# Optimization experiments

Measured on AMD Instinct MI355X. Metric: run time of the kernel, lower is better.

Reference implementation:

```python
import jax, jax.numpy as jnp
import numpy as np
import math

N_LAYER = 4
D = 1024
H = 16
V = 32000
MAX_LEN = 2048
B = 2
L = 2048
EPS = 1e-6


def positional_encoding(max_len, dim):
    pos = jnp.arange(max_len, dtype=jnp.float32)[:, None]
    div = jnp.exp(jnp.arange(0, dim, 2, dtype=jnp.float32) * (-math.log(10000.0) / dim))
    ang = pos * div  # [max_len, dim//2]
    pe = jnp.zeros((max_len, dim), dtype=jnp.float32)
    pe = pe.at[:, 0::2].set(jnp.sin(ang)).at[:, 1::2].set(jnp.cos(ang))
    return pe


def setup_inputs() -> dict:
    key = jax.random.key(0)
    ks = jax.random.split(key, 20)
    s = 0.02
    inp = {
        "input_ids": jax.random.randint(ks[0], (B, L), 0, V),
        "embed": jax.random.normal(ks[1], (V, D), jnp.float32) * s,
        "Wq": jax.random.normal(ks[2], (N_LAYER, D, D), jnp.float32) * s,
        "bq": jnp.zeros((N_LAYER, D), jnp.float32),
        "Wk": jax.random.normal(ks[3], (N_LAYER, D, D), jnp.float32) * s,
        "bk": jnp.zeros((N_LAYER, D), jnp.float32),
        "Wv": jax.random.normal(ks[4], (N_LAYER, D, D), jnp.float32) * s,
        "bv": jnp.zeros((N_LAYER, D), jnp.float32),
        "Wo": jax.random.normal(ks[5], (N_LAYER, D, D), jnp.float32) * s,
        "bo": jnp.zeros((N_LAYER, D), jnp.float32),
        "Wproj": jax.random.normal(ks[6], (N_LAYER, D, 2 * D), jnp.float32) * s,
        "bproj": jnp.zeros((N_LAYER, 2 * D), jnp.float32),
        "Wup": jax.random.normal(ks[7], (N_LAYER, D, 2 * D), jnp.float32) * s,
        "bup": jnp.zeros((N_LAYER, 2 * D), jnp.float32),
        "Wdown": jax.random.normal(ks[8], (N_LAYER, 2 * D, D), jnp.float32) * s,
        "bdown": jnp.zeros((N_LAYER, D), jnp.float32),
        "gammas": jnp.ones((2 * N_LAYER, D), jnp.float32),
        "Wlogits": jax.random.normal(ks[9], (D, V), jnp.float32) * s,
        "blogits": jnp.zeros((V,), jnp.float32),
    }
    return inp


def rmsnorm(x, gamma):
    ms = jnp.mean(x * x, axis=-1, keepdims=True)
    return x * jax.lax.rsqrt(ms + EPS) * gamma


def attention(x, Wq, bq, Wk, bk, Wv, bv, Wo, bo):
    b, l, d = x.shape
    dh = d // H
    q = (x @ Wq + bq).reshape(b, l, H, dh)
    k = (x @ Wk + bk).reshape(b, l, H, dh)
    v = (x @ Wv + bv).reshape(b, l, H, dh)
    scores = jnp.einsum("blhd,bmhd->bhlm", q, k) / math.sqrt(dh)
    causal = jnp.tril(jnp.ones((l, l), dtype=bool))  # True where allowed
    scores = jnp.where(causal, scores, -jnp.inf)
    attn = jax.nn.softmax(scores, axis=-1)
    out = jnp.einsum("bhlm,bmhd->blhd", attn, v).reshape(b, l, d)
    return out @ Wo + bo


def ffn(x, Wproj, bproj, Wup, bup, Wdown, bdown):
    proj = x @ Wproj + bproj
    up = x @ Wup + bup
    gate = jax.nn.silu(proj * up)
    return gate @ Wdown + bdown


def reference(input_ids, embed, Wq, bq, Wk, bk, Wv, bv, Wo, bo,
              Wproj, bproj, Wup, bup, Wdown, bdown, gammas, Wlogits, blogits):
    b, l = input_ids.shape
    pe = positional_encoding(MAX_LEN, D)[:l]
    x = embed[input_ids] + pe
    for i in range(N_LAYER):
        x = x + attention(rmsnorm(x, gammas[2 * i]),
                          Wq[i], bq[i], Wk[i], bk[i], Wv[i], bv[i], Wo[i], bo[i])
        x = x + ffn(rmsnorm(x, gammas[2 * i + 1]),
                    Wproj[i], bproj[i], Wup[i], bup[i], Wdown[i], bdown[i])
    return x @ Wlogits + blogits
```

## Files before the change

### kernel.cpp

```cpp
#include <hip/hip_runtime.h>


typedef _Float16 f16;
typedef _Float16 v8h __attribute__((ext_vector_type(8)));
typedef float    v4f __attribute__((ext_vector_type(4)));

#define B_   2
#define L_   2048
#define D_   1024
#define H_   16
#define V_   32000
#define M_   (B_ * L_)

__device__ inline void g2l16(const void* g, void* l) {
  __builtin_amdgcn_global_load_lds((const __attribute__((address_space(1))) void*)g,
                                   (__attribute__((address_space(3))) void*)l,
                                   16, 0, 0);
}

__device__ inline void xcd_swz(int& bx, int& by, int gx, int gy) {
  int nwg  = gx * gy;
  int orig = by * gx + bx;
  int q = nwg >> 3, r = nwg & 7;
  int xcd = orig & 7, local = orig >> 3;
  int swz = (xcd < r ? xcd * (q + 1) : r * (q + 1) + (xcd - r) * q) + local;
  bx = swz % gx;
  by = swz / gx;
}

template<int EPI>
__global__ __launch_bounds__(256) void gemm_bt(
    const f16* __restrict__ A, const f16* __restrict__ Bt,
    const float* __restrict__ bias, const float* resid, void* outp,
    int N, int K)
{
  __shared__ alignas(16) f16 As[128 * 32];
  __shared__ alignas(16) f16 Bs[128 * 32];

  int bx = blockIdx.x, by = blockIdx.y;
  xcd_swz(bx, by, (int)gridDim.x, (int)gridDim.y);

  const int tid  = threadIdx.x;
  const int wave = tid >> 6, lane = tid & 63;
  const int quad = lane >> 4, l16 = lane & 15;
  const long tm = (long)bx * 128;
  const long tn = (long)by * 128;
  const int wm = (wave >> 1) * 64, wn = (wave & 1) * 64;

  v4f acc[4][4];
  for (int i = 0; i < 4; ++i)
    for (int j = 0; j < 4; ++j)
      for (int r = 0; r < 4; ++r) acc[i][j][r] = 0.f;

  for (int k0 = 0; k0 < K; k0 += 32) {
    __syncthreads();
    for (int h = 0; h < 2; ++h) {
      int c = h * 256 + wave * 64 + lane;
      long row = c >> 2;
      long koff = (long)k0 + (c & 3) * 8;
      g2l16(A  + (tm + row) * K + koff, As + (h * 256 + wave * 64) * 8);
      g2l16(Bt + (tn + row) * K + koff, Bs + (h * 256 + wave * 64) * 8);
    }
    __syncthreads();

    v8h a[4], b[4];
    for (int i = 0; i < 4; ++i) {
      a[i] = *(const v8h*)(As + (wm + i * 16 + l16) * 32 + quad * 8);
      b[i] = *(const v8h*)(Bs + (wn + i * 16 + l16) * 32 + quad * 8);
    }
    for (int i = 0; i < 4; ++i)
      for (int j = 0; j < 4; ++j)
        acc[i][j] = __builtin_amdgcn_mfma_f32_16x16x32_f16(a[i], b[j], acc[i][j], 0, 0, 0);
  }

  for (int i = 0; i < 4; ++i)
    for (int r = 0; r < 4; ++r) {
      long row = tm + wm + i * 16 + quad * 4 + r;
      for (int j = 0; j < 4; ++j) {
        long col = tn + wn + j * 16 + l16;
        float v = acc[i][j][r] + bias[col];
        long idx = row * (long)N + col;
        if (EPI == 0)      ((f16*)outp)[idx] = (f16)v;
        else if (EPI == 1) ((float*)outp)[idx] = resid[idx] + v;
        else               ((float*)outp)[idx] = v;
      }
    }
}

template<int EPI>
__global__ __launch_bounds__(256) void gemm64_bt(
    const f16* __restrict__ A, const f16* __restrict__ Bt,
    const float* __restrict__ bias, const float* resid, void* outp,
    int N, int K)
{
  __shared__ alignas(16) f16 As[128 * 32];
  __shared__ alignas(16) f16 Bs[64 * 32];

  int bx = blockIdx.x, by = blockIdx.y;
  xcd_swz(bx, by, (int)gridDim.x, (int)gridDim.y);

  const int tid  = threadIdx.x;
  const int wave = tid >> 6, lane = tid & 63;
  const int quad = lane >> 4, l16 = lane & 15;
  const long tm = (long)bx * 128;
  const long tn = (long)by * 64;
  const int wm = (wave >> 1) * 64, wn = (wave & 1) * 32;

  v4f acc[4][2];
  for (int i = 0; i < 4; ++i)
    for (int j = 0; j < 2; ++j)
      for (int r = 0; r < 4; ++r) acc[i][j][r] = 0.f;

  for (int k0 = 0; k0 < K; k0 += 32) {
    __syncthreads();
    for (int h = 0; h < 2; ++h) {
      int c = h * 256 + wave * 64 + lane;
      long row = c >> 2;
      long koff = (long)k0 + (c & 3) * 8;
      g2l16(A + (tm + row) * K + koff, As + (h * 256 + wave * 64) * 8);
    }
    {
      int c = wave * 64 + lane;
      long row = c >> 2;
      long koff = (long)k0 + (c & 3) * 8;
      g2l16(Bt + (tn + row) * K + koff, Bs + (wave * 64) * 8);
    }
    __syncthreads();

    v8h a[4], b[2];
    for (int i = 0; i < 4; ++i)
      a[i] = *(const v8h*)(As + (wm + i * 16 + l16) * 32 + quad * 8);
    for (int j = 0; j < 2; ++j)
      b[j] = *(const v8h*)(Bs + (wn + j * 16 + l16) * 32 + quad * 8);
    for (int i = 0; i < 4; ++i)
      for (int j = 0; j < 2; ++j)
        acc[i][j] = __builtin_amdgcn_mfma_f32_16x16x32_f16(a[i], b[j], acc[i][j], 0, 0, 0);
  }

  for (int i = 0; i < 4; ++i)
    for (int r = 0; r < 4; ++r) {
      long row = tm + wm + i * 16 + quad * 4 + r;
      for (int j = 0; j < 2; ++j) {
        long col = tn + wn + j * 16 + l16;
        float v = acc[i][j][r] + bias[col];
        long idx = row * (long)N + col;
        if (EPI == 0)      ((f16*)outp)[idx] = (f16)v;
        else if (EPI == 1) ((float*)outp)[idx] = resid[idx] + v;
        else               ((float*)outp)[idx] = v;
      }
    }
}

__global__ __launch_bounds__(256) void attn_k(const f16* __restrict__ qkv,
                                              f16* __restrict__ attno)
{
  const int qt = (int)gridDim.x - 1 - blockIdx.x;
  const int bh = blockIdx.y;
  const int b = bh >> 4, h = bh & 15;
  const int tid = threadIdx.x;
  const int wave = tid >> 6, lane = tid & 63;
  const int quad = lane >> 4, l16 = lane & 15;

  __shared__ alignas(16) f16 Ks[32 * 64];
  __shared__ alignas(16) f16 Vt[64 * 32];
  __shared__ alignas(16) f16 Ps[4][16 * 32];

  const f16* base = qkv + (size_t)b * L_ * 3072 + h * 64;

  const int qrow = qt * 64 + wave * 16 + l16;
  const v8h qf0 = *(const v8h*)(base + (size_t)qrow * 3072 + quad * 8);
  const v8h qf1 = *(const v8h*)(base + (size_t)qrow * 3072 + 32 + quad * 8);

  v4f of[4];
  float m_i[4], l_i[4];
  for (int n = 0; n < 4; ++n)
    for (int r = 0; r < 4; ++r) of[n][r] = 0.f;
  for (int r = 0; r < 4; ++r) { m_i[r] = -1e30f; l_i[r] = 0.f; }

  const int kr = tid >> 3, kc = tid & 7;
  const int vkr = tid & 31, vkc = tid >> 5;
  const int nblocks = qt * 2 + 2;

  for (int kb = 0; kb < nblocks; ++kb) {
    const int key0 = kb * 32;
    __syncthreads();
    {
      const f16* ksrc = base + 1024 + (size_t)(key0 + kr) * 3072 + kc * 8;
      *(v8h*)(Ks + kr * 64 + ((kc ^ (kr & 7)) * 8)) = *(const v8h*)ksrc;
      const f16* vsrc = base + 2048 + (size_t)(key0 + vkr) * 3072 + vkc * 8;
      v8h vv = *(const v8h*)vsrc;
      const int vc = vkr >> 3, vs = vkr & 7;
      for (int e = 0; e < 8; ++e) {
        int row = vkc * 8 + e;
        Vt[row * 32 + ((vc ^ ((row >> 1) & 3)) * 8) + vs] = vv[e];
      }
    }
    __syncthreads();

    v4f sf[2];
    for (int s = 0; s < 2; ++s)
      for (int r = 0; r < 4; ++r) sf[s][r] = 0.f;
    for (int s = 0; s < 2; ++s) {
      int row = s * 16 + l16;
      v8h kf0 = *(const v8h*)(Ks + row * 64 + ((quad ^ (row & 7)) * 8));
      v8h kf1 = *(const v8h*)(Ks + row * 64 + (((4 + quad) ^ (row & 7)) * 8));
      sf[s] = __builtin_amdgcn_mfma_f32_16x16x32_f16(qf0, kf0, sf[s], 0, 0, 0);
      sf[s] = __builtin_amdgcn_mfma_f32_16x16x32_f16(qf1, kf1, sf[s], 0, 0, 0);
    }

    const int qg0 = qt * 64 + wave * 16 + quad * 4;
    float pv[2][4];
    for (int s = 0; s < 2; ++s)
      for (int r = 0; r < 4; ++r) {
        float sc = sf[s][r] * 0.125f;
        int kg = key0 + s * 16 + l16;
        if (kg > qg0 + r) sc = -1e30f;
        pv[s][r] = sc;
      }

    for (int r = 0; r < 4; ++r) {
      float mx = fmaxf(pv[0][r], pv[1][r]);
      for (int o = 8; o; o >>= 1) mx = fmaxf(mx, __shfl_xor(mx, o, 64));
      float mnew = fmaxf(m_i[r], mx);
      float alpha = expf(m_i[r] - mnew);
      m_i[r] = mnew;
      pv[0][r] = expf(pv[0][r] - mnew);
      pv[1][r] = expf(pv[1][r] - mnew);
      float rs = pv[0][r] + pv[1][r];
      for (int o = 8; o; o >>= 1) rs += __shfl_xor(rs, o, 64);
      l_i[r] = l_i[r] * alpha + rs;
      for (int n = 0; n < 4; ++n) of[n][r] *= alpha;
      Ps[wave][(quad * 4 + r) * 32 + l16]      = (f16)pv[0][r];
      Ps[wave][(quad * 4 + r) * 32 + 16 + l16] = (f16)pv[1][r];
    }
    __syncthreads();

    v8h pf = *(const v8h*)(&Ps[wave][0] + l16 * 32 + quad * 8);
    for (int n = 0; n < 4; ++n) {
      int vrow = n * 16 + l16;
      v8h vf = *(const v8h*)(Vt + vrow * 32 + ((quad ^ ((vrow >> 1) & 3)) * 8));
      of[n] = __builtin_amdgcn_mfma_f32_16x16x32_f16(pf, vf, of[n], 0, 0, 0);
    }
  }

  const int q = qt * 64 + wave * 16 + quad * 4;
  f16* orow = attno + (size_t)b * L_ * 1024 + h * 64;
  for (int r = 0; r < 4; ++r) {
    float inv = 1.0f / l_i[r];
    for (int n = 0; n < 4; ++n)
      orow[(size_t)(q + r) * 1024 + n * 16 + l16] = (f16)(of[n][r] * inv);
  }
}

__global__ __launch_bounds__(256) void embed_pe(const int* __restrict__ ids,
                                                const float* __restrict__ emb,
                                                float* __restrict__ x)
{
  const int bl = blockIdx.x;
  const int l = bl & (L_ - 1);
  const int id = ids[bl];
  const float* e = emb + (size_t)id * D_;
  float* xr = x + (size_t)bl * D_;
  const int d0 = threadIdx.x * 4;
  for (int i = 0; i < 4; ++i) {
    int d = d0 + i;
    int p = d >> 1;
    float ang = (float)l * expf((float)(2 * p) * -0.008994473019508053f);
    float pe = (d & 1) ? cosf(ang) : sinf(ang);
    xr[d] = e[d] + pe;
  }
}

__global__ __launch_bounds__(256) void rmsnorm_k(const float* __restrict__ x,
                                                 const float* __restrict__ gamma,
                                                 f16* __restrict__ y)
{
  const int row = blockIdx.x;
  const float4 v = ((const float4*)(x + (size_t)row * D_))[threadIdx.x];
  float s = v.x * v.x + v.y * v.y + v.z * v.z + v.w * v.w;
  for (int o = 32; o; o >>= 1) s += __shfl_xor(s, o, 64);
  __shared__ float red[4];
  const int wave = threadIdx.x >> 6;
  if ((threadIdx.x & 63) == 0) red[wave] = s;
  __syncthreads();
  const float tot = red[0] + red[1] + red[2] + red[3];
  const float scale = rsqrtf(tot * (1.0f / D_) + 1e-6f);
  f16* yr = y + (size_t)row * D_;
  const int d = threadIdx.x * 4;
  yr[d]     = (f16)(v.x * scale * gamma[d]);
  yr[d + 1] = (f16)(v.y * scale * gamma[d + 1]);
  yr[d + 2] = (f16)(v.z * scale * gamma[d + 2]);
  yr[d + 3] = (f16)(v.w * scale * gamma[d + 3]);
}

__global__ __launch_bounds__(256) void transpose_cvt(const float* __restrict__ in,
                                                     f16* __restrict__ out,
                                                     int K, int N)
{
  __shared__ float tile[32][33];
  const int r = threadIdx.x >> 5, c = threadIdx.x & 31;
  const size_t bk = (size_t)blockIdx.y * 32;
  const size_t bn = (size_t)blockIdx.x * 32;
  for (int i = 0; i < 32; i += 8)
    tile[r + i][c] = in[(bk + r + i) * N + bn + c];
  __syncthreads();
  for (int i = 0; i < 32; i += 8)
    out[(bn + r + i) * K + bk + c] = (f16)tile[c][r + i];
}

__global__ __launch_bounds__(256) void gate_k(const f16* __restrict__ PU,
                                              f16* __restrict__ g)
{
  const int e = (blockIdx.x * 256 + threadIdx.x) * 4;
  const int row = e >> 11, col = e & 2047;
  const f16* p = PU + (size_t)row * 4096 + col;
  const f16* u = p + 2048;
  f16* go = g + (size_t)row * 2048 + col;
  for (int i = 0; i < 4; ++i) {
    float z = (float)p[i] * (float)u[i];
    go[i] = (f16)(z / (1.0f + expf(-z)));
  }
}

__global__ __launch_bounds__(256) void cast_k(const float* __restrict__ x,
                                              f16* __restrict__ y)
{
  const int i = blockIdx.x * 1024 + threadIdx.x * 4;
  const float4 v = *(const float4*)(x + i);
  y[i] = (f16)v.x; y[i + 1] = (f16)v.y; y[i + 2] = (f16)v.z; y[i + 3] = (f16)v.w;
}

__global__ __launch_bounds__(256) void build_biases(
    const float* bq, const float* bk, const float* bv,
    const float* bp, const float* bu, float* bqkv, float* bpu)
{
  const int i = blockIdx.x;
  for (int j = threadIdx.x; j < 3072; j += 256)
    bqkv[i * 3072 + j] = j < 1024 ? bq[i * 1024 + j]
                       : j < 2048 ? bk[i * 1024 + j - 1024]
                                  : bv[i * 1024 + j - 2048];
  for (int j = threadIdx.x; j < 4096; j += 256)
    bpu[i * 4096 + j] = j < 2048 ? bp[i * 2048 + j] : bu[i * 2048 + j - 2048];
}

extern "C" void kernel_launch(void* const* d_in, const int* in_sizes, int n_in,
                              void* d_out, int out_size, void* d_ws, size_t ws_size,
                              hipStream_t stream)
{
  (void)in_sizes; (void)n_in; (void)out_size; (void)ws_size;
  const int*   ids     = (const int*)  d_in[0];
  const float* embed   = (const float*)d_in[1];
  const float* Wq      = (const float*)d_in[2];
  const float* bq      = (const float*)d_in[3];
  const float* Wk      = (const float*)d_in[4];
  const float* bk      = (const float*)d_in[5];
  const float* Wv      = (const float*)d_in[6];
  const float* bv      = (const float*)d_in[7];
  const float* Wo      = (const float*)d_in[8];
  const float* bo      = (const float*)d_in[9];
  const float* Wproj   = (const float*)d_in[10];
  const float* bproj   = (const float*)d_in[11];
  const float* Wup     = (const float*)d_in[12];
  const float* bup     = (const float*)d_in[13];
  const float* Wdown   = (const float*)d_in[14];
  const float* bdown   = (const float*)d_in[15];
  const float* gammas  = (const float*)d_in[16];
  const float* Wlogits = (const float*)d_in[17];
  const float* blogits = (const float*)d_in[18];

  char* ws = (char*)d_ws;
  float* x    = (float*)ws;
  f16*   y    = (f16*)  (ws + 16777216);
  float* bqkv = (float*)(ws + 25165824);
  float* bpu  = (float*)(ws + 25214976);
  f16*   wbuf = (f16*)  (ws + 25280512);
  f16* wqkvT  = wbuf;
  f16* woT    = wbuf + 3145728;
  f16* wpuT   = wbuf + 4194304;
  f16* wdownT = wbuf + 8388608;

  char* ob  = (char*)d_out;
  f16* qkv   = (f16*)ob;
  f16* attno = (f16*)(ob + 25165824);
  f16* PU    = (f16*)(ob + 33554432);
  f16* g     = (f16*)(ob + 67108864);

  embed_pe<<<M_, 256, 0, stream>>>(ids, embed, x);
  build_biases<<<4, 256, 0, stream>>>(bq, bk, bv, bproj, bup, bqkv, bpu);

  for (int i = 0; i < 4; ++i) {
    const float* Wqi = Wq + (size_t)i * 1048576;
    const float* Wki = Wk + (size_t)i * 1048576;
    const float* Wvi = Wv + (size_t)i * 1048576;
    const float* Woi = Wo + (size_t)i * 1048576;
    const float* Wpi = Wproj + (size_t)i * 2097152;
    const float* Wui = Wup   + (size_t)i * 2097152;
    const float* Wdi = Wdown + (size_t)i * 2097152;

    transpose_cvt<<<dim3(32, 32), 256, 0, stream>>>(Wqi, wqkvT,                1024, 1024);
    transpose_cvt<<<dim3(32, 32), 256, 0, stream>>>(Wki, wqkvT + 1048576,      1024, 1024);
    transpose_cvt<<<dim3(32, 32), 256, 0, stream>>>(Wvi, wqkvT + 2097152,      1024, 1024);
    transpose_cvt<<<dim3(32, 32), 256, 0, stream>>>(Woi, woT,                  1024, 1024);
    transpose_cvt<<<dim3(64, 32), 256, 0, stream>>>(Wpi, wpuT,                 1024, 2048);
    transpose_cvt<<<dim3(64, 32), 256, 0, stream>>>(Wui, wpuT + 2097152,       1024, 2048);
    transpose_cvt<<<dim3(32, 64), 256, 0, stream>>>(Wdi, wdownT,               2048, 1024);

    rmsnorm_k<<<M_, 256, 0, stream>>>(x, gammas + (size_t)(2 * i) * 1024, y);
    gemm_bt<0><<<dim3(32, 24), 256, 0, stream>>>(y, wqkvT, bqkv + i * 3072, nullptr, qkv, 3072, 1024);
    attn_k<<<dim3(32, 32), 256, 0, stream>>>(qkv, attno);
    gemm64_bt<1><<<dim3(32, 16), 256, 0, stream>>>(attno, woT, bo + i * 1024, x, x, 1024, 1024);

    rmsnorm_k<<<M_, 256, 0, stream>>>(x, gammas + (size_t)(2 * i + 1) * 1024, y);
    gemm_bt<0><<<dim3(32, 32), 256, 0, stream>>>(y, wpuT, bpu + i * 4096, nullptr, PU, 4096, 1024);
    gate_k<<<8192, 256, 0, stream>>>(PU, g);
    gemm64_bt<1><<<dim3(32, 16), 256, 0, stream>>>(g, wdownT, bdown + i * 1024, x, x, 1024, 2048);
  }

  transpose_cvt<<<dim3(1000, 32), 256, 0, stream>>>(Wlogits, wbuf, 1024, 32000);
  cast_k<<<M_, 256, 0, stream>>>(x, y);
  gemm_bt<2><<<dim3(32, 250), 256, 0, stream>>>(y, wbuf, blogits, nullptr, (float*)d_out, 32000, 1024);
}
```

Before: 2.756 ms.

## Enlarge GEMM tiles to 256x128, swizzle LDS, group tile mapping, widen attention key blocks

The main GEMM moves from 128x128 to 256x128 tiles, so each wave does 8x4 MFMAs per k-step and operands are reused more. Both GEMM kernels now apply an XOR swizzle to LDS rows to avoid bank conflicts, and a grouped, XCD-aware tile mapping improves L2 locality. The attention kernel processes 64 keys per block instead of 32, loads K straight into LDS asynchronously, and uses swizzled layouts for V and P. The larger accumulator raises register pressure and occupancy is capped by launch bounds. With 16x24 blocks the QKV GEMM may leave some CUs idle.

```diff
diff --git a/kernel.cpp b/kernel.cpp
--- a/kernel.cpp
+++ b/kernel.cpp
@@ -18,62 +18,76 @@
                                    16, 0, 0);
 }
 
-__device__ inline void xcd_swz(int& bx, int& by, int gx, int gy) {
-  int nwg  = gx * gy;
-  int orig = by * gx + bx;
-  int q = nwg >> 3, r = nwg & 7;
-  int xcd = orig & 7, local = orig >> 3;
-  int swz = (xcd < r ? xcd * (q + 1) : r * (q + 1) + (xcd - r) * q) + local;
-  bx = swz % gx;
-  by = swz / gx;
+__device__ inline void tile_map(int& m, int& n) {
+  const int GX = (int)gridDim.x, GY = (int)gridDim.y;
+  const int nwg = GX * GY;
+  const int flat = (int)(blockIdx.y * gridDim.x + blockIdx.x);
+  const int per = nwg >> 3, r = nwg & 7;
+  const int xcd = flat & 7, lo = flat >> 3;
+  const int swz = (xcd < r ? xcd * (per + 1) : r * (per + 1) + (xcd - r) * per) + lo;
+  const int MG = 4;
+  const int band = swz / (MG * GY), rem = swz % (MG * GY);
+  n = rem / MG;
+  m = band * MG + (rem % MG);
 }
 
 template<int EPI>
-__global__ __launch_bounds__(256) void gemm_bt(
+__global__ __launch_bounds__(256, 2) void gemm_wt(
     const f16* __restrict__ A, const f16* __restrict__ Bt,
     const float* __restrict__ bias, const float* resid, void* outp,
     int N, int K)
 {
-  __shared__ alignas(16) f16 As[128 * 32];
+  __shared__ alignas(16) f16 As[256 * 32];
   __shared__ alignas(16) f16 Bs[128 * 32];
 
-  int bx = blockIdx.x, by = blockIdx.y;
-  xcd_swz(bx, by, (int)gridDim.x, (int)gridDim.y);
+  int bm, bn;
+  tile_map(bm, bn);
 
   const int tid  = threadIdx.x;
   const int wave = tid >> 6, lane = tid & 63;
   const int quad = lane >> 4, l16 = lane & 15;
-  const long tm = (long)bx * 128;
-  const long tn = (long)by * 128;
-  const int wm = (wave >> 1) * 64, wn = (wave & 1) * 64;
-
-  v4f acc[4][4];
-  for (int i = 0; i < 4; ++i)
+  const long tm = (long)bm * 256;
+  const long tn = (long)bn * 128;
+  const int wm = (wave >> 1) * 128, wn = (wave & 1) * 64;
+
+  v4f acc[8][4];
+  for (int i = 0; i < 8; ++i)
     for (int j = 0; j < 4; ++j)
       for (int r = 0; r < 4; ++r) acc[i][j][r] = 0.f;
 
   for (int k0 = 0; k0 < K; k0 += 32) {
     __syncthreads();
+    for (int h = 0; h < 4; ++h) {
+      int c = h * 256 + tid;
+      long row = c >> 2;
+      int jslot = c & 3;
+      long koff = (long)k0 + ((jslot ^ ((row >> 1) & 3)) << 3);
+      g2l16(A + (tm + row) * K + koff, As + (h * 256 + wave * 64) * 8);
+    }
     for (int h = 0; h < 2; ++h) {
-      int c = h * 256 + wave * 64 + lane;
+      int c = h * 256 + tid;
       long row = c >> 2;
-      long koff = (long)k0 + (c & 3) * 8;
-      g2l16(A  + (tm + row) * K + koff, As + (h * 256 + wave * 64) * 8);
+      int jslot = c & 3;
+      long koff = (long)k0 + ((jslot ^ ((row >> 1) & 3)) << 3);
       g2l16(Bt + (tn + row) * K + koff, Bs + (h * 256 + wave * 64) * 8);
     }
     __syncthreads();
 
-    v8h a[4], b[4];
-    for (int i = 0; i < 4; ++i) {
-      a[i] = *(const v8h*)(As + (wm + i * 16 + l16) * 32 + quad * 8);
-      b[i] = *(const v8h*)(Bs + (wn + i * 16 + l16) * 32 + quad * 8);
-    }
-    for (int i = 0; i < 4; ++i)
+    v8h a[8], b[4];
+    for (int i = 0; i < 8; ++i) {
+      int arow = wm + i * 16 + l16;
+      a[i] = *(const v8h*)(As + arow * 32 + ((quad ^ ((arow >> 1) & 3)) << 3));
+    }
+    for (int j = 0; j < 4; ++j) {
+      int brow = wn + j * 16 + l16;
+      b[j] = *(const v8h*)(Bs + brow * 32 + ((quad ^ ((brow >> 1) & 3)) << 3));
+    }
+    for (int i = 0; i < 8; ++i)
       for (int j = 0; j < 4; ++j)
         acc[i][j] = __builtin_amdgcn_mfma_f32_16x16x32_f16(a[i], b[j], acc[i][j], 0, 0, 0);
   }
 
-  for (int i = 0; i < 4; ++i)
+  for (int i = 0; i < 8; ++i)
     for (int r = 0; r < 4; ++r) {
       long row = tm + wm + i * 16 + quad * 4 + r;
       for (int j = 0; j < 4; ++j) {
@@ -96,14 +110,14 @@
   __shared__ alignas(16) f16 As[128 * 32];
   __shared__ alignas(16) f16 Bs[64 * 32];
 
-  int bx = blockIdx.x, by = blockIdx.y;
-  xcd_swz(bx, by, (int)gridDim.x, (int)gridDim.y);
+  int bm, bn;
+  tile_map(bm, bn);
 
   const int tid  = threadIdx.x;
   const int wave = tid >> 6, lane = tid & 63;
   const int quad = lane >> 4, l16 = lane & 15;
-  const long tm = (long)bx * 128;
-  const long tn = (long)by * 64;
+  const long tm = (long)bm * 128;
+  const long tn = (long)bn * 64;
   const int wm = (wave >> 1) * 64, wn = (wave & 1) * 32;
 
   v4f acc[4][2];
@@ -114,24 +128,30 @@
   for (int k0 = 0; k0 < K; k0 += 32) {
     __syncthreads();
     for (int h = 0; h < 2; ++h) {
-      int c = h * 256 + wave * 64 + lane;
+      int c = h * 256 + tid;
       long row = c >> 2;
-      long koff = (long)k0 + (c & 3) * 8;
+      int jslot = c & 3;
+      long koff = (long)k0 + ((jslot ^ ((row >> 1) & 3)) << 3);
       g2l16(A + (tm + row) * K + koff, As + (h * 256 + wave * 64) * 8);
     }
     {
-      int c = wave * 64 + lane;
+      int c = tid;
       long row = c >> 2;
-      long koff = (long)k0 + (c & 3) * 8;
+      int jslot = c & 3;
+      long koff = (long)k0 + ((jslot ^ ((row >> 1) & 3)) << 3);
       g2l16(Bt + (tn + row) * K + koff, Bs + (wave * 64) * 8);
     }
     __syncthreads();
 
     v8h a[4], b[2];
-    for (int i = 0; i < 4; ++i)
-      a[i] = *(const v8h*)(As + (wm + i * 16 + l16) * 32 + quad * 8);
-    for (int j = 0; j < 2; ++j)
-      b[j] = *(const v8h*)(Bs + (wn + j * 16 + l16) * 32 + quad * 8);
+    for (int i = 0; i < 4; ++i) {
+      int arow = wm + i * 16 + l16;
+      a[i] = *(const v8h*)(As + arow * 32 + ((quad ^ ((arow >> 1) & 3)) << 3));
+    }
+    for (int j = 0; j < 2; ++j) {
+      int brow = wn + j * 16 + l16;
+      b[j] = *(const v8h*)(Bs + brow * 32 + ((quad ^ ((brow >> 1) & 3)) << 3));
+    }
     for (int i = 0; i < 4; ++i)
       for (int j = 0; j < 2; ++j)
         acc[i][j] = __builtin_amdgcn_mfma_f32_16x16x32_f16(a[i], b[j], acc[i][j], 0, 0, 0);
@@ -161,9 +181,9 @@
   const int wave = tid >> 6, lane = tid & 63;
   const int quad = lane >> 4, l16 = lane & 15;
 
-  __shared__ alignas(16) f16 Ks[32 * 64];
-  __shared__ alignas(16) f16 Vt[64 * 32];
-  __shared__ alignas(16) f16 Ps[4][16 * 32];
+  __shared__ alignas(16) f16 Ks[64 * 64];
+  __shared__ alignas(16) f16 Vt[64 * 64];
+  __shared__ alignas(16) f16 Ps[4][16 * 64];
 
   const f16* base = qkv + (size_t)b * L_ * 3072 + h * 64;
 
@@ -177,40 +197,44 @@
     for (int r = 0; r < 4; ++r) of[n][r] = 0.f;
   for (int r = 0; r < 4; ++r) { m_i[r] = -1e30f; l_i[r] = 0.f; }
 
-  const int kr = tid >> 3, kc = tid & 7;
-  const int vkr = tid & 31, vkc = tid >> 5;
-  const int nblocks = qt * 2 + 2;
+  const int nblocks = qt + 1;
 
   for (int kb = 0; kb < nblocks; ++kb) {
-    const int key0 = kb * 32;
-    __syncthreads();
-    {
-      const f16* ksrc = base + 1024 + (size_t)(key0 + kr) * 3072 + kc * 8;
-      *(v8h*)(Ks + kr * 64 + ((kc ^ (kr & 7)) * 8)) = *(const v8h*)ksrc;
-      const f16* vsrc = base + 2048 + (size_t)(key0 + vkr) * 3072 + vkc * 8;
+    const int key0 = kb * 64;
+    __syncthreads();
+    for (int h2 = 0; h2 < 2; ++h2) {
+      int c = h2 * 256 + tid;
+      int row = c >> 3, jslot = c & 7;
+      const f16* ksrc = base + 1024 + (size_t)(key0 + row) * 3072
+                        + ((jslot ^ (row & 7)) << 3);
+      g2l16(ksrc, Ks + (h2 * 256 + wave * 64) * 8);
+    }
+    for (int h2 = 0; h2 < 2; ++h2) {
+      int key = tid >> 2;
+      int dc = (tid & 3) + h2 * 4;
+      const f16* vsrc = base + 2048 + (size_t)(key0 + key) * 3072 + dc * 8;
       v8h vv = *(const v8h*)vsrc;
-      const int vc = vkr >> 3, vs = vkr & 7;
       for (int e = 0; e < 8; ++e) {
-        int row = vkc * 8 + e;
-        Vt[row * 32 + ((vc ^ ((row >> 1) & 3)) * 8) + vs] = vv[e];
-      }
-    }
-    __syncthreads();
-
-    v4f sf[2];
-    for (int s = 0; s < 2; ++s)
+        int d = dc * 8 + e;
+        Vt[d * 64 + (((key >> 3) ^ (d & 7)) << 3) + (key & 7)] = vv[e];
+      }
+    }
+    __syncthreads();
+
+    v4f sf[4];
+    for (int s = 0; s < 4; ++s)
       for (int r = 0; r < 4; ++r) sf[s][r] = 0.f;
-    for (int s = 0; s < 2; ++s) {
-      int row = s * 16 + l16;
-      v8h kf0 = *(const v8h*)(Ks + row * 64 + ((quad ^ (row & 7)) * 8));
-      v8h kf1 = *(const v8h*)(Ks + row * 64 + (((4 + quad) ^ (row & 7)) * 8));
+    for (int s = 0; s < 4; ++s) {
+      int krow = s * 16 + l16;
+      v8h kf0 = *(const v8h*)(Ks + krow * 64 + ((quad       ^ (krow & 7)) << 3));
+      v8h kf1 = *(const v8h*)(Ks + krow * 64 + (((4 + quad) ^ (krow & 7)) << 3));
       sf[s] = __builtin_amdgcn_mfma_f32_16x16x32_f16(qf0, kf0, sf[s], 0, 0, 0);
       sf[s] = __builtin_amdgcn_mfma_f32_16x16x32_f16(qf1, kf1, sf[s], 0, 0, 0);
     }
 
     const int qg0 = qt * 64 + wave * 16 + quad * 4;
-    float pv[2][4];
-    for (int s = 0; s < 2; ++s)
+    float pv[4][4];
+    for (int s = 0; s < 4; ++s)
       for (int r = 0; r < 4; ++r) {
         float sc = sf[s][r] * 0.125f;
         int kg = key0 + s * 16 + l16;
@@ -219,27 +243,36 @@
       }
 
     for (int r = 0; r < 4; ++r) {
-      float mx = fmaxf(pv[0][r], pv[1][r]);
+      float mx = fmaxf(fmaxf(pv[0][r], pv[1][r]), fmaxf(pv[2][r], pv[3][r]));
       for (int o = 8; o; o >>= 1) mx = fmaxf(mx, __shfl_xor(mx, o, 64));
       float mnew = fmaxf(m_i[r], mx);
       float alpha = expf(m_i[r] - mnew);
       m_i[r] = mnew;
-      pv[0][r] = expf(pv[0][r] - mnew);
-      pv[1][r] = expf(pv[1][r] - mnew);
-      float rs = pv[0][r] + pv[1][r];
+      float rs = 0.f;
+      for (int s = 0; s < 4; ++s) {
+        pv[s][r] = expf(pv[s][r] - mnew);
+        rs += pv[s][r];
+      }
       for (int o = 8; o; o >>= 1) rs += __shfl_xor(rs, o, 64);
       l_i[r] = l_i[r] * alpha + rs;
       for (int n = 0; n < 4; ++n) of[n][r] *= alpha;
-      Ps[wave][(quad * 4 + r) * 32 + l16]      = (f16)pv[0][r];
-      Ps[wave][(quad * 4 + r) * 32 + 16 + l16] = (f16)pv[1][r];
-    }
-    __syncthreads();
-
-    v8h pf = *(const v8h*)(&Ps[wave][0] + l16 * 32 + quad * 8);
+      int qr = quad * 4 + r;
+      for (int s = 0; s < 4; ++s) {
+        int key = s * 16 + l16;
+        Ps[wave][qr * 64 + ((((key >> 3)) ^ (qr & 7)) << 3) + (key & 7)]
+            = (f16)pv[s][r];
+      }
+    }
+    __syncthreads();
+
+    v8h pf0 = *(const v8h*)(&Ps[wave][0] + l16 * 64 + ((quad       ^ (l16 & 7)) << 3));
+    v8h pf1 = *(const v8h*)(&Ps[wave][0] + l16 * 64 + (((4 + quad) ^ (l16 & 7)) << 3));
     for (int n = 0; n < 4; ++n) {
-      int vrow = n * 16 + l16;
-      v8h vf = *(const v8h*)(Vt + vrow * 32 + ((quad ^ ((vrow >> 1) & 3)) * 8));
-      of[n] = __builtin_amdgcn_mfma_f32_16x16x32_f16(pf, vf, of[n], 0, 0, 0);
+      int d = n * 16 + l16;
+      v8h vf0 = *(const v8h*)(Vt + d * 64 + ((quad       ^ (d & 7)) << 3));
+      v8h vf1 = *(const v8h*)(Vt + d * 64 + (((4 + quad) ^ (d & 7)) << 3));
+      of[n] = __builtin_amdgcn_mfma_f32_16x16x32_f16(pf0, vf0, of[n], 0, 0, 0);
+      of[n] = __builtin_amdgcn_mfma_f32_16x16x32_f16(pf1, vf1, of[n], 0, 0, 0);
     }
   }
 
@@ -406,17 +439,17 @@
     transpose_cvt<<<dim3(32, 64), 256, 0, stream>>>(Wdi, wdownT,               2048, 1024);
 
     rmsnorm_k<<<M_, 256, 0, stream>>>(x, gammas + (size_t)(2 * i) * 1024, y);
-    gemm_bt<0><<<dim3(32, 24), 256, 0, stream>>>(y, wqkvT, bqkv + i * 3072, nullptr, qkv, 3072, 1024);
+    gemm_wt<0><<<dim3(16, 24), 256, 0, stream>>>(y, wqkvT, bqkv + i * 3072, nullptr, qkv, 3072, 1024);
     attn_k<<<dim3(32, 32), 256, 0, stream>>>(qkv, attno);
     gemm64_bt<1><<<dim3(32, 16), 256, 0, stream>>>(attno, woT, bo + i * 1024, x, x, 1024, 1024);
 
     rmsnorm_k<<<M_, 256, 0, stream>>>(x, gammas + (size_t)(2 * i + 1) * 1024, y);
-    gemm_bt<0><<<dim3(32, 32), 256, 0, stream>>>(y, wpuT, bpu + i * 4096, nullptr, PU, 4096, 1024);
+    gemm_wt<0><<<dim3(16, 32), 256, 0, stream>>>(y, wpuT, bpu + i * 4096, nullptr, PU, 4096, 1024);
     gate_k<<<8192, 256, 0, stream>>>(PU, g);
     gemm64_bt<1><<<dim3(32, 16), 256, 0, stream>>>(g, wdownT, bdown + i * 1024, x, x, 1024, 2048);
   }
 
   transpose_cvt<<<dim3(1000, 32), 256, 0, stream>>>(Wlogits, wbuf, 1024, 32000);
   cast_k<<<M_, 256, 0, stream>>>(x, y);
-  gemm_bt<2><<<dim3(32, 250), 256, 0, stream>>>(y, wbuf, blogits, nullptr, (float*)d_out, 32000, 1024);
-}
+  gemm_wt<2><<<dim3(16, 250), 256, 0, stream>>>(y, wbuf, blogits, nullptr, (float*)d_out, 32000, 1024);
+}
```

After: 2.527 ms. 1.09x faster.
